# Optimization experiments

Hardware: AMD Instinct MI355X
Metric: run time of the kernel (lower is better)

Reference implementation:

```python
import jax, jax.numpy as jnp
import numpy as np

B, T, I, H, C = 64, 2048, 256, 256, 10


def setup_inputs() -> dict:
    key = jax.random.key(0)
    ks = jax.random.split(key, 8)
    s_i = 1.0 / np.sqrt(H)
    return {
        "x": jax.random.normal(ks[0], (B, T, I), dtype=jnp.float32),
        "key_mat": jax.random.normal(ks[1], (I, I), dtype=jnp.float32) * (1.0 / np.sqrt(I)),
        "W_ih": jax.random.uniform(ks[2], (4 * H, I), jnp.float32, -s_i, s_i),
        "W_hh": jax.random.uniform(ks[3], (4 * H, H), jnp.float32, -s_i, s_i),
        "b_ih": jax.random.uniform(ks[4], (4 * H,), jnp.float32, -s_i, s_i),
        "b_hh": jax.random.uniform(ks[5], (4 * H,), jnp.float32, -s_i, s_i),
        "W_cls": jax.random.uniform(ks[6], (C, H), jnp.float32, -s_i, s_i),
        "b_cls": jax.random.uniform(ks[7], (C,), jnp.float32, -s_i, s_i),
    }


def reference(x, key_mat, W_ih, W_hh, b_ih, b_hh, W_cls, b_cls):
    # Keyed LSTM: each timestep input is multiplied by the key matrix before
    # the standard LSTM gate computation. Applying the key per step is
    # mathematically identical to one batched matmul up front.
    xk = jnp.einsum("bti,ij->btj", x, key_mat)              # [B,T,I]
    # Precompute input projections for all timesteps (gate order: i,f,g,o)
    x_proj = jnp.einsum("btj,gj->btg", xk, W_ih) + b_ih      # [B,T,4H]

    def step(carry, xt):
        h, c = carry
        gates = xt + h @ W_hh.T + b_hh                        # [B,4H]
        i_g, f_g, g_g, o_g = jnp.split(gates, 4, axis=-1)
        i_g = jax.nn.sigmoid(i_g)
        f_g = jax.nn.sigmoid(f_g)
        g_g = jnp.tanh(g_g)
        o_g = jax.nn.sigmoid(o_g)
        c = f_g * c + i_g * g_g
        h = o_g * jnp.tanh(c)
        return (h, c), None

    h0 = jnp.zeros((x.shape[0], W_hh.shape[1]), x.dtype)
    (h_last, _), _ = jax.lax.scan(step, (h0, h0), jnp.swapaxes(x_proj, 0, 1))
    return h_last @ W_cls.T + b_cls                           # [B,C]
```

## Files before the change

### kernel.cpp

```cpp
#include <hip/hip_runtime.h>
#include <hip/hip_bf16.h>
#include <stdint.h>

#define BB   64
#define TT   2048
#define II   256
#define HH   256
#define G4   1024
#define NC   10

typedef _Float16 half2v __attribute__((ext_vector_type(2)));
typedef _Float16 half8v __attribute__((ext_vector_type(8)));
typedef float    float4v __attribute__((ext_vector_type(4)));

__device__ __forceinline__ float fdot2(uint32_t w, uint32_t h, float acc) {
  return __builtin_amdgcn_fdot2(__builtin_bit_cast(half2v, w),
                                __builtin_bit_cast(half2v, h), acc, false);
}
__device__ __forceinline__ float sigmf(float v) { return 1.f / (1.f + __expf(-v)); }
__device__ __forceinline__ float tanhf2(float v) { float e = __expf(2.f * v); return 1.f - 2.f / (e + 1.f); }

__device__ __forceinline__ void bar_lds() {
  asm volatile("s_waitcnt lgkmcnt(0)\n\ts_barrier" ::: "memory");
}

__global__ __launch_bounds__(1024) void prep_wc(
    const float* __restrict__ key, const float* __restrict__ Wih,
    const float* __restrict__ bih, const float* __restrict__ bhh,
    _Float16* __restrict__ WcT, float* __restrict__ biasc) {
  __shared__ float krow[II];
  const int i = blockIdx.x;
  const int g = threadIdx.x;
  if (g < II) krow[g] = key[(size_t)i * II + g];
  __syncthreads();
  const float4* w4 = (const float4*)(Wih + (size_t)g * II);
  float acc = 0.f;
#pragma unroll 8
  for (int j = 0; j < II / 4; ++j) {
    float4 w = w4[j];
    acc += w.x * krow[4 * j] + w.y * krow[4 * j + 1] + w.z * krow[4 * j + 2] + w.w * krow[4 * j + 3];
  }
  WcT[(size_t)g * II + i] = (_Float16)acc;
  if (i == 0) biasc[g] = bih[g] + bhh[g];
}

__global__ __launch_bounds__(256) void prep_whh(
    const float* __restrict__ Whh, uint32_t* __restrict__ wrg, uint32_t* __restrict__ wld) {
  const int id = blockIdx.x * 256 + threadIdx.x;
  const int g  = id & (G4 - 1);
  const int kp = id >> 10;
  float a = Whh[(size_t)g * HH + 2 * kp];
  float b = Whh[(size_t)g * HH + 2 * kp + 1];
  half2v h = {(_Float16)a, (_Float16)b};
  uint32_t packed = __builtin_bit_cast(uint32_t, h);
  if (kp < 112) {
    wrg[kp * G4 + g] = packed;
  } else {
    const int t = g & 511, hh = g >> 9;
    const int d = kp - 112;
    const int c = hh * 4 + (d >> 2), j = d & 3;
    wld[(size_t)(c * 512 + t) * 4 + j] = packed;
  }
}

__global__ __launch_bounds__(256) void gemm_xproj(
    const float* __restrict__ x, const _Float16* __restrict__ WcT,
    const float* __restrict__ biasc, _Float16* __restrict__ xpk) {
  __shared__ __align__(16) _Float16 Asm[128][40];
  __shared__ __align__(16) _Float16 Bsm[128][40];
  const int t = threadIdx.x;
  const int n0 = blockIdx.x * 128;
  const int m0 = blockIdx.y * 128;
  const int r = t >> 1;
  const int hoff = (t & 1) * 16;
  const int lane = t & 63, wave = t >> 6;
  const int quad = lane >> 4, l15 = lane & 15;
  const int mh = (wave & 1) * 64, nh = (wave >> 1) * 64;
  float4v zero = {0.f, 0.f, 0.f, 0.f};
  float4v acc[4][4];
#pragma unroll
  for (int a = 0; a < 4; ++a)
#pragma unroll
    for (int b = 0; b < 4; ++b) acc[a][b] = zero;

  for (int kt = 0; kt < 8; ++kt) {
    const int k0 = kt * 32;
    const float4* xa = (const float4*)(x + (size_t)(m0 + r) * II + k0 + hoff);
    float4 f0 = xa[0], f1 = xa[1], f2 = xa[2], f3 = xa[3];
    half8v lo = {(_Float16)f0.x, (_Float16)f0.y, (_Float16)f0.z, (_Float16)f0.w,
                 (_Float16)f1.x, (_Float16)f1.y, (_Float16)f1.z, (_Float16)f1.w};
    half8v hi = {(_Float16)f2.x, (_Float16)f2.y, (_Float16)f2.z, (_Float16)f2.w,
                 (_Float16)f3.x, (_Float16)f3.y, (_Float16)f3.z, (_Float16)f3.w};
    const half8v* bsrc = (const half8v*)(WcT + (size_t)(n0 + r) * II + k0 + hoff);
    half8v b0 = bsrc[0], b1 = bsrc[1];
    *(half8v*)&Asm[r][hoff]     = lo;
    *(half8v*)&Asm[r][hoff + 8] = hi;
    *(half8v*)&Bsm[r][hoff]     = b0;
    *(half8v*)&Bsm[r][hoff + 8] = b1;
    __syncthreads();
    half8v af[4], bf[4];
#pragma unroll
    for (int mt = 0; mt < 4; ++mt) af[mt] = *(const half8v*)&Asm[mh + mt * 16 + l15][quad * 8];
#pragma unroll
    for (int nt = 0; nt < 4; ++nt) bf[nt] = *(const half8v*)&Bsm[nh + nt * 16 + l15][quad * 8];
#pragma unroll
    for (int mt = 0; mt < 4; ++mt)
#pragma unroll
      for (int nt = 0; nt < 4; ++nt)
        acc[mt][nt] = __builtin_amdgcn_mfma_f32_16x16x32_f16(af[mt], bf[nt], acc[mt][nt], 0, 0, 0);
    __syncthreads();
  }
  _Float16* dst = xpk;
#pragma unroll
  for (int nt = 0; nt < 4; ++nt) {
    const int col = n0 + nh + nt * 16 + l15;
    const float bias = biasc[col];
    const int cslot = (col & 511) * 2 + (col >> 9);
#pragma unroll
    for (int mt = 0; mt < 4; ++mt) {
      const int mrow = m0 + mh + mt * 16 + quad * 4;
#pragma unroll
      for (int j = 0; j < 4; ++j)
        dst[(size_t)(mrow + j) * 1024 + cslot] = (_Float16)(acc[mt][nt][j] + bias);
    }
  }
}

__global__ __launch_bounds__(512, 2) void lstm_seq(
    const uint32_t* __restrict__ xpk, const uint32_t* __restrict__ wrg,
    const uint4* __restrict__ wld, float* __restrict__ hfin) {
  __shared__ __align__(16) uint4 wsm[8 * 512];
  __shared__ __align__(16) uint32_t hsm[128];
  __shared__ float gsm[512];
  const int t0 = threadIdx.x, t1 = t0 + 512, b = blockIdx.x;

  uint32_t w0[112], w1[112];
#pragma unroll
  for (int c = 0; c < 112; ++c) { w0[c] = wrg[c * G4 + t0]; w1[c] = wrg[c * G4 + t1]; }
#pragma unroll
  for (int c = 0; c < 8; ++c) wsm[c * 512 + t0] = wld[c * 512 + t0];
  if (t0 < 128) hsm[t0] = 0;
  float cst = 0.f, hlast = 0.f;
  const uint32_t* xp = xpk + (size_t)b * TT * 512 + t0;
  uint32_t xn = xp[0];
  __syncthreads();

  for (int t = 0; t < TT; ++t) {
    const uint32_t xw = xn;
    xn = xp[(size_t)((t < TT - 1) ? t + 1 : t) * 512];
    float a00 = 0.f, a01 = 0.f, a10 = 0.f, a11 = 0.f;
    const uint4* h4 = (const uint4*)hsm;
#pragma unroll
    for (int cc = 0; cc < 28; ++cc) {
      uint4 hc = h4[cc];
      a00 = fdot2(w0[4 * cc + 0], hc.x, a00);
      a01 = fdot2(w0[4 * cc + 1], hc.y, a01);
      a00 = fdot2(w0[4 * cc + 2], hc.z, a00);
      a01 = fdot2(w0[4 * cc + 3], hc.w, a01);
      a10 = fdot2(w1[4 * cc + 0], hc.x, a10);
      a11 = fdot2(w1[4 * cc + 1], hc.y, a11);
      a10 = fdot2(w1[4 * cc + 2], hc.z, a10);
      a11 = fdot2(w1[4 * cc + 3], hc.w, a11);
    }
#pragma unroll
    for (int j = 0; j < 4; ++j) {
      uint4 hc = h4[28 + j];
      uint4 wa = wsm[j * 512 + t0];
      uint4 wb = wsm[(4 + j) * 512 + t0];
      a00 = fdot2(wa.x, hc.x, a00);
      a01 = fdot2(wa.y, hc.y, a01);
      a00 = fdot2(wa.z, hc.z, a00);
      a01 = fdot2(wa.w, hc.w, a01);
      a10 = fdot2(wb.x, hc.x, a10);
      a11 = fdot2(wb.y, hc.y, a11);
      a10 = fdot2(wb.z, hc.z, a10);
      a11 = fdot2(wb.w, hc.w, a11);
    }
    half2v xh = __builtin_bit_cast(half2v, xw);
    const float s0 = (a00 + a01) + (float)xh.x;
    const float s1 = (a10 + a11) + (float)xh.y;
    if (t0 >= 256) { gsm[t0 - 256] = s0; gsm[t0] = s1; }
    bar_lds();
    if (t0 < 256) {
      float ig = sigmf(s0);
      float gg = tanhf2(s1);
      float fg = sigmf(gsm[t0]);
      float og = sigmf(gsm[t0 + 256]);
      cst = fg * cst + ig * gg;
      hlast = og * tanhf2(cst);
      ((_Float16*)hsm)[t0] = (_Float16)hlast;
    }
    bar_lds();
  }
  if (t0 < 256) hfin[(size_t)b * HH + t0] = hlast;
}

__global__ __launch_bounds__(256) void cls_k(
    const float* __restrict__ hfin, const float* __restrict__ Wcls,
    const float* __restrict__ bcls, float* __restrict__ out) {
  __shared__ float part[4][NC];
  const int b = blockIdx.x, tid = threadIdx.x;
  const int lane = tid & 63, wave = tid >> 6;
  float hv = hfin[(size_t)b * HH + tid];
#pragma unroll
  for (int c = 0; c < NC; ++c) {
    float p = hv * Wcls[c * HH + tid];
#pragma unroll
    for (int off = 32; off >= 1; off >>= 1) p += __shfl_down(p, off, 64);
    if (lane == 0) part[wave][c] = p;
  }
  __syncthreads();
  if (tid < NC) {
    out[(size_t)b * NC + tid] =
        part[0][tid] + part[1][tid] + part[2][tid] + part[3][tid] + bcls[tid];
  }
}

extern "C" void kernel_launch(void* const* d_in, const int* in_sizes, int n_in,
                              void* d_out, int out_size, void* d_ws, size_t ws_size,
                              hipStream_t stream) {
  (void)in_sizes; (void)n_in; (void)out_size; (void)ws_size;
  const float* x    = (const float*)d_in[0];
  const float* key  = (const float*)d_in[1];
  const float* Wih  = (const float*)d_in[2];
  const float* Whh  = (const float*)d_in[3];
  const float* bih  = (const float*)d_in[4];
  const float* bhh  = (const float*)d_in[5];
  const float* Wcls = (const float*)d_in[6];
  const float* bcls = (const float*)d_in[7];
  float* out = (float*)d_out;

  char* ws = (char*)d_ws;
  size_t off = 0;
  uint32_t* xpk  = (uint32_t*)(ws + off); off += (size_t)BB * TT * 512 * 4;
  uint32_t* wrg  = (uint32_t*)(ws + off); off += (size_t)112 * G4 * 4;
  uint32_t* wld  = (uint32_t*)(ws + off); off += (size_t)8 * 512 * 16;
  _Float16* WcT  = (_Float16*)(ws + off); off += (size_t)G4 * II * 2;
  float* biasc   = (float*)(ws + off);    off += (size_t)G4 * 4;
  float* hfin    = (float*)(ws + off);    off += (size_t)BB * HH * 4;

  hipLaunchKernelGGL(prep_wc,  dim3(II),  dim3(G4),  0, stream, key, Wih, bih, bhh, WcT, biasc);
  hipLaunchKernelGGL(prep_whh, dim3(512), dim3(256), 0, stream, Whh, wrg, wld);
  hipLaunchKernelGGL(gemm_xproj, dim3(G4 / 128, (BB * TT) / 128), dim3(256), 0, stream,
                     x, WcT, biasc, (_Float16*)xpk);
  hipLaunchKernelGGL(lstm_seq, dim3(BB), dim3(512), 0, stream, xpk, wrg, (const uint4*)wld, hfin);
  hipLaunchKernelGGL(cls_k,    dim3(BB), dim3(256), 0, stream, hfin, Wcls, bcls, out);
}
```

Before: 4.484 ms.

## Compute all four gates per thread in LSTM step with readlane h broadcast

The recurrent kernel moves from 512 threads each computing two gate rows to 256 threads each computing all four gates of one hidden unit. That removes the gate exchange through shared memory and one of the two per-step barriers. The hidden state is double-buffered in LDS and broadcast across the wave with readlane instead of per-thread LDS vector loads. W_hh and the x-projection layouts are re-packed so each thread reads its four gates contiguously. The cost is about 416 weight registers per thread, which risks spills or very low occupancy, plus many scalar readlane operations in the inner loop.

```diff
diff --git a/kernel.cpp b/kernel.cpp
--- a/kernel.cpp
+++ b/kernel.cpp
@@ -8,6 +8,8 @@
 #define HH   256
 #define G4   1024
 #define NC   10
+#define KREG 104
+#define KLDS (128 - KREG)
 
 typedef _Float16 half2v __attribute__((ext_vector_type(2)));
 typedef _Float16 half8v __attribute__((ext_vector_type(8)));
@@ -53,13 +55,11 @@
   float b = Whh[(size_t)g * HH + 2 * kp + 1];
   half2v h = {(_Float16)a, (_Float16)b};
   uint32_t packed = __builtin_bit_cast(uint32_t, h);
-  if (kp < 112) {
-    wrg[kp * G4 + g] = packed;
+  const int j = g & 255, q = g >> 8;
+  if (kp < KREG) {
+    wrg[((size_t)kp * 256 + j) * 4 + q] = packed;
   } else {
-    const int t = g & 511, hh = g >> 9;
-    const int d = kp - 112;
-    const int c = hh * 4 + (d >> 2), j = d & 3;
-    wld[(size_t)(c * 512 + t) * 4 + j] = packed;
+    wld[((size_t)(kp - KREG) * 256 + j) * 4 + q] = packed;
   }
 }
 
@@ -115,84 +115,90 @@
   for (int nt = 0; nt < 4; ++nt) {
     const int col = n0 + nh + nt * 16 + l15;
     const float bias = biasc[col];
-    const int cslot = (col & 511) * 2 + (col >> 9);
+    const int slot16 = (col & 255) * 4 + (col >> 8);
 #pragma unroll
     for (int mt = 0; mt < 4; ++mt) {
       const int mrow = m0 + mh + mt * 16 + quad * 4;
 #pragma unroll
       for (int j = 0; j < 4; ++j)
-        dst[(size_t)(mrow + j) * 1024 + cslot] = (_Float16)(acc[mt][nt][j] + bias);
+        dst[(size_t)(mrow + j) * 1024 + slot16] = (_Float16)(acc[mt][nt][j] + bias);
     }
   }
 }
 
-__global__ __launch_bounds__(512, 2) void lstm_seq(
-    const uint32_t* __restrict__ xpk, const uint32_t* __restrict__ wrg,
+__global__ __launch_bounds__(256, 1) void lstm_seq(
+    const uint32_t* __restrict__ xpk, const uint4* __restrict__ wrg,
     const uint4* __restrict__ wld, float* __restrict__ hfin) {
-  __shared__ __align__(16) uint4 wsm[8 * 512];
-  __shared__ __align__(16) uint32_t hsm[128];
-  __shared__ float gsm[512];
-  const int t0 = threadIdx.x, t1 = t0 + 512, b = blockIdx.x;
-
-  uint32_t w0[112], w1[112];
-#pragma unroll
-  for (int c = 0; c < 112; ++c) { w0[c] = wrg[c * G4 + t0]; w1[c] = wrg[c * G4 + t1]; }
-#pragma unroll
-  for (int c = 0; c < 8; ++c) wsm[c * 512 + t0] = wld[c * 512 + t0];
-  if (t0 < 128) hsm[t0] = 0;
+  __shared__ __align__(16) uint4 wsm[KLDS * 256];
+  __shared__ __align__(16) uint32_t hsm[256];
+  const int j = threadIdx.x, b = blockIdx.x;
+  const int lane = j & 63;
+
+  uint32_t w[4 * KREG];
+#pragma unroll
+  for (int kp = 0; kp < KREG; ++kp) {
+    uint4 v = wrg[(size_t)kp * 256 + j];
+    w[4 * kp + 0] = v.x; w[4 * kp + 1] = v.y; w[4 * kp + 2] = v.z; w[4 * kp + 3] = v.w;
+  }
+#pragma unroll
+  for (int c = 0; c < KLDS; ++c) wsm[c * 256 + j] = wld[c * 256 + j];
+  if (j < 128) hsm[j] = 0;
   float cst = 0.f, hlast = 0.f;
-  const uint32_t* xp = xpk + (size_t)b * TT * 512 + t0;
-  uint32_t xn = xp[0];
+  const uint2* xq = (const uint2*)xpk + (size_t)b * TT * 256 + j;
+  uint2 xn = xq[0];
   __syncthreads();
 
   for (int t = 0; t < TT; ++t) {
-    const uint32_t xw = xn;
-    xn = xp[(size_t)((t < TT - 1) ? t + 1 : t) * 512];
-    float a00 = 0.f, a01 = 0.f, a10 = 0.f, a11 = 0.f;
-    const uint4* h4 = (const uint4*)hsm;
-#pragma unroll
-    for (int cc = 0; cc < 28; ++cc) {
-      uint4 hc = h4[cc];
-      a00 = fdot2(w0[4 * cc + 0], hc.x, a00);
-      a01 = fdot2(w0[4 * cc + 1], hc.y, a01);
-      a00 = fdot2(w0[4 * cc + 2], hc.z, a00);
-      a01 = fdot2(w0[4 * cc + 3], hc.w, a01);
-      a10 = fdot2(w1[4 * cc + 0], hc.x, a10);
-      a11 = fdot2(w1[4 * cc + 1], hc.y, a11);
-      a10 = fdot2(w1[4 * cc + 2], hc.z, a10);
-      a11 = fdot2(w1[4 * cc + 3], hc.w, a11);
+    const uint2 xw = xn;
+    xn = xq[(size_t)((t + 1) & (TT - 1)) * 256];
+    uint2 hh2 = *(const uint2*)&hsm[(t & 1) * 128 + 2 * lane];
+    uint32_t hv0 = hh2.x, hv1 = hh2.y;
+    float a0 = 0.f, a1 = 0.f, a2 = 0.f, a3 = 0.f;
+#pragma unroll
+    for (int cc = 0; cc < KREG / 4; ++cc) {
+      uint32_t hx = __builtin_amdgcn_readlane(hv0, 2 * cc);
+      uint32_t hy = __builtin_amdgcn_readlane(hv1, 2 * cc);
+      uint32_t hz = __builtin_amdgcn_readlane(hv0, 2 * cc + 1);
+      uint32_t hw = __builtin_amdgcn_readlane(hv1, 2 * cc + 1);
+      a0 = fdot2(w[(4 * cc + 0) * 4 + 0], hx, a0);
+      a1 = fdot2(w[(4 * cc + 0) * 4 + 1], hx, a1);
+      a2 = fdot2(w[(4 * cc + 0) * 4 + 2], hx, a2);
+      a3 = fdot2(w[(4 * cc + 0) * 4 + 3], hx, a3);
+      a0 = fdot2(w[(4 * cc + 1) * 4 + 0], hy, a0);
+      a1 = fdot2(w[(4 * cc + 1) * 4 + 1], hy, a1);
+      a2 = fdot2(w[(4 * cc + 1) * 4 + 2], hy, a2);
+      a3 = fdot2(w[(4 * cc + 1) * 4 + 3], hy, a3);
+      a0 = fdot2(w[(4 * cc + 2) * 4 + 0], hz, a0);
+      a1 = fdot2(w[(4 * cc + 2) * 4 + 1], hz, a1);
+      a2 = fdot2(w[(4 * cc + 2) * 4 + 2], hz, a2);
+      a3 = fdot2(w[(4 * cc + 2) * 4 + 3], hz, a3);
+      a0 = fdot2(w[(4 * cc + 3) * 4 + 0], hw, a0);
+      a1 = fdot2(w[(4 * cc + 3) * 4 + 1], hw, a1);
+      a2 = fdot2(w[(4 * cc + 3) * 4 + 2], hw, a2);
+      a3 = fdot2(w[(4 * cc + 3) * 4 + 3], hw, a3);
     }
 #pragma unroll
-    for (int j = 0; j < 4; ++j) {
-      uint4 hc = h4[28 + j];
-      uint4 wa = wsm[j * 512 + t0];
-      uint4 wb = wsm[(4 + j) * 512 + t0];
-      a00 = fdot2(wa.x, hc.x, a00);
-      a01 = fdot2(wa.y, hc.y, a01);
-      a00 = fdot2(wa.z, hc.z, a00);
-      a01 = fdot2(wa.w, hc.w, a01);
-      a10 = fdot2(wb.x, hc.x, a10);
-      a11 = fdot2(wb.y, hc.y, a11);
-      a10 = fdot2(wb.z, hc.z, a10);
-      a11 = fdot2(wb.w, hc.w, a11);
+    for (int kk = 0; kk < KLDS; ++kk) {
+      uint32_t h = (kk & 1) ? __builtin_amdgcn_readlane(hv1, (KREG >> 1) + (kk >> 1))
+                            : __builtin_amdgcn_readlane(hv0, (KREG >> 1) + (kk >> 1));
+      uint4 wv = wsm[kk * 256 + j];
+      a0 = fdot2(wv.x, h, a0);
+      a1 = fdot2(wv.y, h, a1);
+      a2 = fdot2(wv.z, h, a2);
+      a3 = fdot2(wv.w, h, a3);
     }
-    half2v xh = __builtin_bit_cast(half2v, xw);
-    const float s0 = (a00 + a01) + (float)xh.x;
-    const float s1 = (a10 + a11) + (float)xh.y;
-    if (t0 >= 256) { gsm[t0 - 256] = s0; gsm[t0] = s1; }
+    half2v xa = __builtin_bit_cast(half2v, xw.x);
+    half2v xb = __builtin_bit_cast(half2v, xw.y);
+    float ig = sigmf(a0 + (float)xa.x);
+    float fg = sigmf(a1 + (float)xa.y);
+    float gg = tanhf2(a2 + (float)xb.x);
+    float og = sigmf(a3 + (float)xb.y);
+    cst = fg * cst + ig * gg;
+    hlast = og * tanhf2(cst);
+    ((_Float16*)hsm)[((t + 1) & 1) * 256 + j] = (_Float16)hlast;
     bar_lds();
-    if (t0 < 256) {
-      float ig = sigmf(s0);
-      float gg = tanhf2(s1);
-      float fg = sigmf(gsm[t0]);
-      float og = sigmf(gsm[t0 + 256]);
-      cst = fg * cst + ig * gg;
-      hlast = og * tanhf2(cst);
-      ((_Float16*)hsm)[t0] = (_Float16)hlast;
-    }
-    bar_lds();
-  }
-  if (t0 < 256) hfin[(size_t)b * HH + t0] = hlast;
+  }
+  hfin[(size_t)b * HH + j] = hlast;
 }
 
 __global__ __launch_bounds__(256) void cls_k(
@@ -233,8 +239,8 @@
   char* ws = (char*)d_ws;
   size_t off = 0;
   uint32_t* xpk  = (uint32_t*)(ws + off); off += (size_t)BB * TT * 512 * 4;
-  uint32_t* wrg  = (uint32_t*)(ws + off); off += (size_t)112 * G4 * 4;
-  uint32_t* wld  = (uint32_t*)(ws + off); off += (size_t)8 * 512 * 16;
+  uint32_t* wrg  = (uint32_t*)(ws + off); off += (size_t)KREG * 256 * 16;
+  uint32_t* wld  = (uint32_t*)(ws + off); off += (size_t)KLDS * 256 * 16;
   _Float16* WcT  = (_Float16*)(ws + off); off += (size_t)G4 * II * 2;
   float* biasc   = (float*)(ws + off);    off += (size_t)G4 * 4;
   float* hfin    = (float*)(ws + off);    off += (size_t)BB * HH * 4;
@@ -243,6 +249,7 @@
   hipLaunchKernelGGL(prep_whh, dim3(512), dim3(256), 0, stream, Whh, wrg, wld);
   hipLaunchKernelGGL(gemm_xproj, dim3(G4 / 128, (BB * TT) / 128), dim3(256), 0, stream,
                      x, WcT, biasc, (_Float16*)xpk);
-  hipLaunchKernelGGL(lstm_seq, dim3(BB), dim3(512), 0, stream, xpk, wrg, (const uint4*)wld, hfin);
+  hipLaunchKernelGGL(lstm_seq, dim3(BB), dim3(256), 0, stream,
+                     xpk, (const uint4*)wrg, (const uint4*)wld, hfin);
   hipLaunchKernelGGL(cls_k,    dim3(BB), dim3(256), 0, stream, hfin, Wcls, bcls, out);
 }
```

Measured after the change: 6.716 ms. 49.8% more time.

## Compute recurrent h·W_hh with MFMA fragments instead of fdot2 dot products

Applied to the files above, without the earlier changes.

The per-step recurrent matvec moves from scalar fdot2 accumulation to 16x16x32 f16 MFMA instructions. W_hh is pre-packed into MFMA A-fragments: six k-tiles live in registers and two in LDS. The h vector is broadcast as the B operand, and one lane per column group writes the gate pre-activations to LDS. The x-projection layout is changed to four gates per hidden unit so each thread reads one uint2. The intent is fewer issued instructions per step, at the cost of wasted MFMA columns (15 of 16 outputs are redundant) and higher MFMA latency on the serial chain.

```diff
diff --git a/kernel.cpp b/kernel.cpp
--- a/kernel.cpp
+++ b/kernel.cpp
@@ -13,10 +13,6 @@
 typedef _Float16 half8v __attribute__((ext_vector_type(8)));
 typedef float    float4v __attribute__((ext_vector_type(4)));
 
-__device__ __forceinline__ float fdot2(uint32_t w, uint32_t h, float acc) {
-  return __builtin_amdgcn_fdot2(__builtin_bit_cast(half2v, w),
-                                __builtin_bit_cast(half2v, h), acc, false);
-}
 __device__ __forceinline__ float sigmf(float v) { return 1.f / (1.f + __expf(-v)); }
 __device__ __forceinline__ float tanhf2(float v) { float e = __expf(2.f * v); return 1.f - 2.f / (e + 1.f); }
 
@@ -44,23 +40,21 @@
   if (i == 0) biasc[g] = bih[g] + bhh[g];
 }
 
-__global__ __launch_bounds__(256) void prep_whh(
-    const float* __restrict__ Whh, uint32_t* __restrict__ wrg, uint32_t* __restrict__ wld) {
+__global__ __launch_bounds__(256) void prep_wfrag(
+    const float* __restrict__ Whh, uint4* __restrict__ wreg, uint4* __restrict__ wldsG) {
   const int id = blockIdx.x * 256 + threadIdx.x;
-  const int g  = id & (G4 - 1);
-  const int kp = id >> 10;
-  float a = Whh[(size_t)g * HH + 2 * kp];
-  float b = Whh[(size_t)g * HH + 2 * kp + 1];
-  half2v h = {(_Float16)a, (_Float16)b};
-  uint32_t packed = __builtin_bit_cast(uint32_t, h);
-  if (kp < 112) {
-    wrg[kp * G4 + g] = packed;
-  } else {
-    const int t = g & 511, hh = g >> 9;
-    const int d = kp - 112;
-    const int c = hh * 4 + (d >> 2), j = d & 3;
-    wld[(size_t)(c * 512 + t) * 4 + j] = packed;
-  }
+  const int lane = id & 63;
+  const int m  = (id >> 6) & 7;
+  const int w  = (id >> 9) & 7;
+  const int kt = (id >> 12) & 7;
+  const int row = w * 128 + m * 16 + (lane & 15);
+  const int k0  = kt * 32 + (lane >> 4) * 8;
+  half8v frag;
+#pragma unroll
+  for (int jj = 0; jj < 8; ++jj) frag[jj] = (_Float16)Whh[(size_t)row * HH + k0 + jj];
+  uint4 u = __builtin_bit_cast(uint4, frag);
+  if (kt < 6) wreg[((kt * 8 + w) * 8 + m) * 64 + lane] = u;
+  else        wldsG[(((kt - 6) * 8 + w) * 8 + m) * 64 + lane] = u;
 }
 
 __global__ __launch_bounds__(256) void gemm_xproj(
@@ -115,80 +109,81 @@
   for (int nt = 0; nt < 4; ++nt) {
     const int col = n0 + nh + nt * 16 + l15;
     const float bias = biasc[col];
-    const int cslot = (col & 511) * 2 + (col >> 9);
+    const int slot16 = (col & 255) * 4 + (col >> 8);
 #pragma unroll
     for (int mt = 0; mt < 4; ++mt) {
       const int mrow = m0 + mh + mt * 16 + quad * 4;
 #pragma unroll
       for (int j = 0; j < 4; ++j)
-        dst[(size_t)(mrow + j) * 1024 + cslot] = (_Float16)(acc[mt][nt][j] + bias);
+        dst[(size_t)(mrow + j) * 1024 + slot16] = (_Float16)(acc[mt][nt][j] + bias);
     }
   }
 }
 
 __global__ __launch_bounds__(512, 2) void lstm_seq(
-    const uint32_t* __restrict__ xpk, const uint32_t* __restrict__ wrg,
-    const uint4* __restrict__ wld, float* __restrict__ hfin) {
-  __shared__ __align__(16) uint4 wsm[8 * 512];
-  __shared__ __align__(16) uint32_t hsm[128];
-  __shared__ float gsm[512];
-  const int t0 = threadIdx.x, t1 = t0 + 512, b = blockIdx.x;
-
-  uint32_t w0[112], w1[112];
-#pragma unroll
-  for (int c = 0; c < 112; ++c) { w0[c] = wrg[c * G4 + t0]; w1[c] = wrg[c * G4 + t1]; }
-#pragma unroll
-  for (int c = 0; c < 8; ++c) wsm[c * 512 + t0] = wld[c * 512 + t0];
-  if (t0 < 128) hsm[t0] = 0;
+    const uint32_t* __restrict__ xpk, const uint4* __restrict__ wreg,
+    const uint4* __restrict__ wldsG, float* __restrict__ hfin) {
+  __shared__ __align__(16) _Float16 wsmh[2 * 8 * 8 * 64 * 8];
+  __shared__ __align__(16) _Float16 hsh[256];
+  __shared__ __align__(16) float gsh[G4];
+  const int t0 = threadIdx.x, b = blockIdx.x;
+  const int w = t0 >> 6, lane = t0 & 63, quad = lane >> 4;
+
+  half8v wA[48];
+#pragma unroll
+  for (int kt = 0; kt < 6; ++kt)
+#pragma unroll
+    for (int m = 0; m < 8; ++m)
+      wA[kt * 8 + m] = __builtin_bit_cast(half8v, wreg[((kt * 8 + w) * 8 + m) * 64 + lane]);
+#pragma unroll
+  for (int i = 0; i < 16; ++i)
+    ((uint4*)wsmh)[i * 512 + t0] = wldsG[i * 512 + t0];
+  if (t0 < 128) ((uint32_t*)hsh)[t0] = 0;
+
   float cst = 0.f, hlast = 0.f;
-  const uint32_t* xp = xpk + (size_t)b * TT * 512 + t0;
-  uint32_t xn = xp[0];
+  const uint2* xq = (const uint2*)xpk + (size_t)b * TT * 256 + t0;
+  uint2 xn = {0u, 0u};
+  if (t0 < 256) xn = xq[0];
   __syncthreads();
 
+  const float4v zero = {0.f, 0.f, 0.f, 0.f};
   for (int t = 0; t < TT; ++t) {
-    const uint32_t xw = xn;
-    xn = xp[(size_t)((t < TT - 1) ? t + 1 : t) * 512];
-    float a00 = 0.f, a01 = 0.f, a10 = 0.f, a11 = 0.f;
-    const uint4* h4 = (const uint4*)hsm;
-#pragma unroll
-    for (int cc = 0; cc < 28; ++cc) {
-      uint4 hc = h4[cc];
-      a00 = fdot2(w0[4 * cc + 0], hc.x, a00);
-      a01 = fdot2(w0[4 * cc + 1], hc.y, a01);
-      a00 = fdot2(w0[4 * cc + 2], hc.z, a00);
-      a01 = fdot2(w0[4 * cc + 3], hc.w, a01);
-      a10 = fdot2(w1[4 * cc + 0], hc.x, a10);
-      a11 = fdot2(w1[4 * cc + 1], hc.y, a11);
-      a10 = fdot2(w1[4 * cc + 2], hc.z, a10);
-      a11 = fdot2(w1[4 * cc + 3], hc.w, a11);
-    }
-#pragma unroll
-    for (int j = 0; j < 4; ++j) {
-      uint4 hc = h4[28 + j];
-      uint4 wa = wsm[j * 512 + t0];
-      uint4 wb = wsm[(4 + j) * 512 + t0];
-      a00 = fdot2(wa.x, hc.x, a00);
-      a01 = fdot2(wa.y, hc.y, a01);
-      a00 = fdot2(wa.z, hc.z, a00);
-      a01 = fdot2(wa.w, hc.w, a01);
-      a10 = fdot2(wb.x, hc.x, a10);
-      a11 = fdot2(wb.y, hc.y, a11);
-      a10 = fdot2(wb.z, hc.z, a10);
-      a11 = fdot2(wb.w, hc.w, a11);
-    }
-    half2v xh = __builtin_bit_cast(half2v, xw);
-    const float s0 = (a00 + a01) + (float)xh.x;
-    const float s1 = (a10 + a11) + (float)xh.y;
-    if (t0 >= 256) { gsm[t0 - 256] = s0; gsm[t0] = s1; }
+    const uint2 xw = xn;
+    if (t0 < 256) xn = xq[(size_t)((t + 1) & (TT - 1)) * 256];
+    float4v acc[8];
+#pragma unroll
+    for (int kt = 0; kt < 8; ++kt) {
+      half8v bf = *(const half8v*)&hsh[kt * 32 + quad * 8];
+      if (kt < 6) {
+#pragma unroll
+        for (int m = 0; m < 8; ++m)
+          acc[m] = __builtin_amdgcn_mfma_f32_16x16x32_f16(
+              wA[kt * 8 + m], bf, (kt == 0) ? zero : acc[m], 0, 0, 0);
+      } else {
+#pragma unroll
+        for (int m = 0; m < 8; ++m) {
+          half8v wf = *(const half8v*)&wsmh[((((kt - 6) * 8 + w) * 8 + m) * 64 + lane) * 8];
+          acc[m] = __builtin_amdgcn_mfma_f32_16x16x32_f16(wf, bf, acc[m], 0, 0, 0);
+        }
+      }
+    }
+    if ((lane & 15) == 0) {
+#pragma unroll
+      for (int m = 0; m < 8; ++m)
+        *(float4v*)&gsh[w * 128 + m * 16 + quad * 4] = acc[m];
+    }
     bar_lds();
     if (t0 < 256) {
-      float ig = sigmf(s0);
-      float gg = tanhf2(s1);
-      float fg = sigmf(gsm[t0]);
-      float og = sigmf(gsm[t0 + 256]);
-      cst = fg * cst + ig * gg;
+      float gi = gsh[t0], gf = gsh[t0 + 256], gg = gsh[t0 + 512], go = gsh[t0 + 768];
+      half2v xa = __builtin_bit_cast(half2v, xw.x);
+      half2v xb = __builtin_bit_cast(half2v, xw.y);
+      float ig = sigmf(gi + (float)xa.x);
+      float fg = sigmf(gf + (float)xa.y);
+      float g2 = tanhf2(gg + (float)xb.x);
+      float og = sigmf(go + (float)xb.y);
+      cst = fg * cst + ig * g2;
       hlast = og * tanhf2(cst);
-      ((_Float16*)hsm)[t0] = (_Float16)hlast;
+      hsh[t0] = (_Float16)hlast;
     }
     bar_lds();
   }
@@ -233,16 +228,17 @@
   char* ws = (char*)d_ws;
   size_t off = 0;
   uint32_t* xpk  = (uint32_t*)(ws + off); off += (size_t)BB * TT * 512 * 4;
-  uint32_t* wrg  = (uint32_t*)(ws + off); off += (size_t)112 * G4 * 4;
-  uint32_t* wld  = (uint32_t*)(ws + off); off += (size_t)8 * 512 * 16;
+  uint4* wreg    = (uint4*)(ws + off);    off += (size_t)6 * 8 * 8 * 64 * 16;
+  uint4* wldsG   = (uint4*)(ws + off);    off += (size_t)2 * 8 * 8 * 64 * 16;
   _Float16* WcT  = (_Float16*)(ws + off); off += (size_t)G4 * II * 2;
   float* biasc   = (float*)(ws + off);    off += (size_t)G4 * 4;
   float* hfin    = (float*)(ws + off);    off += (size_t)BB * HH * 4;
 
-  hipLaunchKernelGGL(prep_wc,  dim3(II),  dim3(G4),  0, stream, key, Wih, bih, bhh, WcT, biasc);
-  hipLaunchKernelGGL(prep_whh, dim3(512), dim3(256), 0, stream, Whh, wrg, wld);
+  hipLaunchKernelGGL(prep_wc,   dim3(II),  dim3(G4),  0, stream, key, Wih, bih, bhh, WcT, biasc);
+  hipLaunchKernelGGL(prep_wfrag, dim3(128), dim3(256), 0, stream, Whh, wreg, wldsG);
   hipLaunchKernelGGL(gemm_xproj, dim3(G4 / 128, (BB * TT) / 128), dim3(256), 0, stream,
                      x, WcT, biasc, (_Float16*)xpk);
-  hipLaunchKernelGGL(lstm_seq, dim3(BB), dim3(512), 0, stream, xpk, wrg, (const uint4*)wld, hfin);
+  hipLaunchKernelGGL(lstm_seq, dim3(BB), dim3(512), 0, stream,
+                     xpk, wreg, wldsG, hfin);
   hipLaunchKernelGGL(cls_k,    dim3(BB), dim3(256), 0, stream, hfin, Wcls, bcls, out);
 }
```

Result: no change. 4.535 ms (+1.1%).

## Use one thread per gate row with readlane broadcast of hidden state

Applied to the files above, without the earlier changes.

The recurrent LSTM kernel now launches 1024 threads per block so that each thread owns one gate row instead of two. Weights are split between 92 register columns and 36 LDS columns. The hidden state is loaded once per lane and broadcast with readlane instead of repeated LDS vector reads. Gate activations are spread across all four thread quarters before the cell update, which shortens the per-step serial chain at the cost of a larger block, more barrier participants, and more LDS for weights.

```diff
diff --git a/kernel.cpp b/kernel.cpp
--- a/kernel.cpp
+++ b/kernel.cpp
@@ -8,6 +8,8 @@
 #define HH   256
 #define G4   1024
 #define NC   10
+#define KREG 92
+#define KTL  (128 - KREG)
 
 typedef _Float16 half2v __attribute__((ext_vector_type(2)));
 typedef _Float16 half8v __attribute__((ext_vector_type(8)));
@@ -53,13 +55,11 @@
   float b = Whh[(size_t)g * HH + 2 * kp + 1];
   half2v h = {(_Float16)a, (_Float16)b};
   uint32_t packed = __builtin_bit_cast(uint32_t, h);
-  if (kp < 112) {
+  if (kp < KREG) {
     wrg[kp * G4 + g] = packed;
   } else {
-    const int t = g & 511, hh = g >> 9;
-    const int d = kp - 112;
-    const int c = hh * 4 + (d >> 2), j = d & 3;
-    wld[(size_t)(c * 512 + t) * 4 + j] = packed;
+    const int d = kp - KREG;
+    wld[((size_t)(d >> 2) * G4 + g) * 4 + (d & 3)] = packed;
   }
 }
 
@@ -126,66 +126,65 @@
   }
 }
 
-__global__ __launch_bounds__(512, 2) void lstm_seq(
+__global__ __launch_bounds__(1024, 4) void lstm_seq(
     const uint32_t* __restrict__ xpk, const uint32_t* __restrict__ wrg,
     const uint4* __restrict__ wld, float* __restrict__ hfin) {
-  __shared__ __align__(16) uint4 wsm[8 * 512];
+  __shared__ __align__(16) uint4 wsm[9 * G4];
   __shared__ __align__(16) uint32_t hsm[128];
-  __shared__ float gsm[512];
-  const int t0 = threadIdx.x, t1 = t0 + 512, b = blockIdx.x;
-
-  uint32_t w0[112], w1[112];
-#pragma unroll
-  for (int c = 0; c < 112; ++c) { w0[c] = wrg[c * G4 + t0]; w1[c] = wrg[c * G4 + t1]; }
-#pragma unroll
-  for (int c = 0; c < 8; ++c) wsm[c * 512 + t0] = wld[c * 512 + t0];
+  __shared__ float gsm[768];
+  const int t0 = threadIdx.x, b = blockIdx.x;
+  const int lane = t0 & 63;
+  const int q = t0 >> 8;
+  const int k = t0 & 255;
+
+  uint32_t w[KREG];
+#pragma unroll
+  for (int c = 0; c < KREG; ++c) w[c] = wrg[c * G4 + t0];
+#pragma unroll
+  for (int c = 0; c < 9; ++c) wsm[c * G4 + t0] = wld[c * G4 + t0];
   if (t0 < 128) hsm[t0] = 0;
-  float cst = 0.f, hlast = 0.f;
-  const uint32_t* xp = xpk + (size_t)b * TT * 512 + t0;
+  float cst = 0.f, hlast = 0.f, ig = 0.f;
+  const uint32_t* xp = xpk + (size_t)b * TT * 512 + (t0 & 511);
   uint32_t xn = xp[0];
   __syncthreads();
 
   for (int t = 0; t < TT; ++t) {
     const uint32_t xw = xn;
     xn = xp[(size_t)((t < TT - 1) ? t + 1 : t) * 512];
-    float a00 = 0.f, a01 = 0.f, a10 = 0.f, a11 = 0.f;
-    const uint4* h4 = (const uint4*)hsm;
-#pragma unroll
-    for (int cc = 0; cc < 28; ++cc) {
-      uint4 hc = h4[cc];
-      a00 = fdot2(w0[4 * cc + 0], hc.x, a00);
-      a01 = fdot2(w0[4 * cc + 1], hc.y, a01);
-      a00 = fdot2(w0[4 * cc + 2], hc.z, a00);
-      a01 = fdot2(w0[4 * cc + 3], hc.w, a01);
-      a10 = fdot2(w1[4 * cc + 0], hc.x, a10);
-      a11 = fdot2(w1[4 * cc + 1], hc.y, a11);
-      a10 = fdot2(w1[4 * cc + 2], hc.z, a10);
-      a11 = fdot2(w1[4 * cc + 3], hc.w, a11);
-    }
-#pragma unroll
-    for (int j = 0; j < 4; ++j) {
-      uint4 hc = h4[28 + j];
-      uint4 wa = wsm[j * 512 + t0];
-      uint4 wb = wsm[(4 + j) * 512 + t0];
-      a00 = fdot2(wa.x, hc.x, a00);
-      a01 = fdot2(wa.y, hc.y, a01);
-      a00 = fdot2(wa.z, hc.z, a00);
-      a01 = fdot2(wa.w, hc.w, a01);
-      a10 = fdot2(wb.x, hc.x, a10);
-      a11 = fdot2(wb.y, hc.y, a11);
-      a10 = fdot2(wb.z, hc.z, a10);
-      a11 = fdot2(wb.w, hc.w, a11);
+    uint2 hh2 = *(const uint2*)&hsm[2 * lane];
+    uint32_t hv0 = hh2.x, hv1 = hh2.y;
+    float a0 = 0.f, a1 = 0.f;
+#pragma unroll
+    for (int cc = 0; cc < KREG / 4; ++cc) {
+      uint32_t hx = __builtin_amdgcn_readlane(hv0, 2 * cc);
+      uint32_t hy = __builtin_amdgcn_readlane(hv1, 2 * cc);
+      uint32_t hz = __builtin_amdgcn_readlane(hv0, 2 * cc + 1);
+      uint32_t hw = __builtin_amdgcn_readlane(hv1, 2 * cc + 1);
+      a0 = fdot2(w[4 * cc + 0], hx, a0);
+      a1 = fdot2(w[4 * cc + 1], hy, a1);
+      a0 = fdot2(w[4 * cc + 2], hz, a0);
+      a1 = fdot2(w[4 * cc + 3], hw, a1);
+    }
+#pragma unroll
+    for (int j = 0; j < 9; ++j) {
+      uint32_t hx = __builtin_amdgcn_readlane(hv0, (KREG >> 1) + 2 * j);
+      uint32_t hy = __builtin_amdgcn_readlane(hv1, (KREG >> 1) + 2 * j);
+      uint32_t hz = __builtin_amdgcn_readlane(hv0, (KREG >> 1) + 2 * j + 1);
+      uint32_t hw = __builtin_amdgcn_readlane(hv1, (KREG >> 1) + 2 * j + 1);
+      uint4 wa = wsm[j * G4 + t0];
+      a0 = fdot2(wa.x, hx, a0);
+      a1 = fdot2(wa.y, hy, a1);
+      a0 = fdot2(wa.z, hz, a0);
+      a1 = fdot2(wa.w, hw, a1);
     }
     half2v xh = __builtin_bit_cast(half2v, xw);
-    const float s0 = (a00 + a01) + (float)xh.x;
-    const float s1 = (a10 + a11) + (float)xh.y;
-    if (t0 >= 256) { gsm[t0 - 256] = s0; gsm[t0] = s1; }
+    const float s = (a0 + a1) + (float)((t0 < 512) ? xh.x : xh.y);
+    if (q == 0)      ig = sigmf(s);
+    else if (q == 2) gsm[256 + k] = tanhf2(s);
+    else             gsm[(q == 1 ? 0 : 512) + k] = sigmf(s);
     bar_lds();
     if (t0 < 256) {
-      float ig = sigmf(s0);
-      float gg = tanhf2(s1);
-      float fg = sigmf(gsm[t0]);
-      float og = sigmf(gsm[t0 + 256]);
+      float fg = gsm[t0], gg = gsm[256 + t0], og = gsm[512 + t0];
       cst = fg * cst + ig * gg;
       hlast = og * tanhf2(cst);
       ((_Float16*)hsm)[t0] = (_Float16)hlast;
@@ -233,8 +232,8 @@
   char* ws = (char*)d_ws;
   size_t off = 0;
   uint32_t* xpk  = (uint32_t*)(ws + off); off += (size_t)BB * TT * 512 * 4;
-  uint32_t* wrg  = (uint32_t*)(ws + off); off += (size_t)112 * G4 * 4;
-  uint32_t* wld  = (uint32_t*)(ws + off); off += (size_t)8 * 512 * 16;
+  uint32_t* wrg  = (uint32_t*)(ws + off); off += (size_t)KREG * G4 * 4;
+  uint32_t* wld  = (uint32_t*)(ws + off); off += (size_t)9 * G4 * 16;
   _Float16* WcT  = (_Float16*)(ws + off); off += (size_t)G4 * II * 2;
   float* biasc   = (float*)(ws + off);    off += (size_t)G4 * 4;
   float* hfin    = (float*)(ws + off);    off += (size_t)BB * HH * 4;
@@ -243,6 +242,6 @@
   hipLaunchKernelGGL(prep_whh, dim3(512), dim3(256), 0, stream, Whh, wrg, wld);
   hipLaunchKernelGGL(gemm_xproj, dim3(G4 / 128, (BB * TT) / 128), dim3(256), 0, stream,
                      x, WcT, biasc, (_Float16*)xpk);
-  hipLaunchKernelGGL(lstm_seq, dim3(BB), dim3(512), 0, stream, xpk, wrg, (const uint4*)wld, hfin);
+  hipLaunchKernelGGL(lstm_seq, dim3(BB), dim3(1024), 0, stream, xpk, wrg, (const uint4*)wld, hfin);
   hipLaunchKernelGGL(cls_k,    dim3(BB), dim3(256), 0, stream, hfin, Wcls, bcls, out);
 }
```

Result: slower. 4.994 ms (+11.4%).
